# Kernel tuning notes

Measured on AMD Instinct MI355X. Metric: run time of the kernel, lower is better.

The kernel has to match this reference:

```python
import jax, jax.numpy as jnp
import numpy as np

D_MODEL = 1024
N_HEADS = 16
D_K = 64
D_FF = 4 * D_MODEL
LN_EPS = 1e-5


def _ln(x, g, b):
    mu = jnp.mean(x, axis=-1, keepdims=True)
    var = jnp.mean((x - mu) ** 2, axis=-1, keepdims=True)
    return (x - mu) * jax.lax.rsqrt(var + LN_EPS) * g + b


def setup_inputs() -> dict:
    key = jax.random.key(0)
    ks = jax.random.split(key, 24)
    d, h, dk, dff = D_MODEL, N_HEADS, D_K, D_FF
    s = lambda k, sh, fan: jax.random.normal(k, sh, jnp.float32) / np.sqrt(fan)
    return {
        "x": jax.random.normal(ks[0], (2, 2048, d), jnp.float32),
        "mask": jnp.ones((2, 2048), jnp.int32),
        # pre-attention q/k/v embed linears (d -> d)
        "Wqe": s(ks[1], (d, d), d), "bqe": jnp.zeros((d,), jnp.float32),
        "Wke": s(ks[2], (d, d), d), "bke": jnp.zeros((d,), jnp.float32),
        "Wve": s(ks[3], (d, d), d), "bve": jnp.zeros((d,), jnp.float32),
        # MHA projections (d -> h*dk) and output fc
        "Wq": s(ks[4], (d, h * dk), d), "bq": jnp.zeros((h * dk,), jnp.float32),
        "Wk": s(ks[5], (d, h * dk), d), "bk": jnp.zeros((h * dk,), jnp.float32),
        "Wv": s(ks[6], (d, h * dk), d), "bv": jnp.zeros((h * dk,), jnp.float32),
        "Wo": s(ks[7], (h * dk, d), h * dk), "bo": jnp.zeros((d,), jnp.float32),
        # layer norms
        "g1": jnp.ones((d,), jnp.float32), "b1": jnp.zeros((d,), jnp.float32),
        "g2": jnp.ones((d,), jnp.float32), "b2": jnp.zeros((d,), jnp.float32),
        # FFN
        "W1": s(ks[8], (d, dff), d), "bb1": jnp.zeros((dff,), jnp.float32),
        "W2": s(ks[9], (dff, d), dff), "bb2": jnp.zeros((d,), jnp.float32),
    }


def reference(x, mask, Wqe, bqe, Wke, bke, Wve, bve, Wq, bq, Wk, bk, Wv, bv,
              Wo, bo, g1, b1, g2, b2, W1, bb1, W2, bb2):
    N, T, _ = x.shape
    h, dk = N_HEADS, D_K
    # pre-embeds then MHA projections
    q = ((x @ Wqe + bqe) @ Wq + bq).reshape(N, T, h, dk)
    k = ((x @ Wke + bke) @ Wk + bk).reshape(N, T, h, dk)
    v = ((x @ Wve + bve) @ Wv + bv).reshape(N, T, h, dk)
    scores = jnp.einsum("bthd,bshd->bhts", q, k) / np.sqrt(dk).astype(np.float32)
    scores = jnp.where(mask[:, None, None, :] == 0, -jnp.inf, scores)
    attn = jax.nn.softmax(scores, axis=-1)
    a = jnp.einsum("bhts,bshd->bthd", attn, v).reshape(N, T, h * dk)
    mha_out = a @ Wo + bo
    x = _ln(x + mha_out, g1, b1)
    ffn = jax.nn.gelu(x @ W1 + bb1, approximate=False) @ W2 + bb2
    x = _ln(x + ffn, g2, b2)
    return x  # dropout is identity in eval mode
```

## Files before the change

### kernel.cpp

```cpp
#include <hip/hip_runtime.h>
#include <stdint.h>
#include <math.h>


#define DM   1024
#define DFF  4096
#define NH   16
#define DKH  64
#define TSEQ 2048
#define TOK  4096

using f32x4  = float  __attribute__((ext_vector_type(4)));
using bf16x8 = __bf16 __attribute__((ext_vector_type(8)));
using s16x8  = short  __attribute__((ext_vector_type(8)));

typedef const void __attribute__((address_space(1)))* gas_ptr;
typedef void       __attribute__((address_space(3)))* las_ptr;

__device__ __forceinline__ short f2bf(float f) {
  unsigned u; __builtin_memcpy(&u, &f, 4);
  u += 0x7FFFu + ((u >> 16) & 1u);
  return (short)(u >> 16);
}
__device__ __forceinline__ float bf2f(short s) {
  unsigned u = ((unsigned)(unsigned short)s) << 16;
  float f; __builtin_memcpy(&f, &u, 4);
  return f;
}
__device__ __forceinline__ unsigned cvt_pk_bf16(float lo, float hi) {
  unsigned r;
  asm volatile("v_cvt_pk_bf16_f32 %0, %1, %2" : "=v"(r) : "v"(lo), "v"(hi));
  return r;
}
__device__ __forceinline__ f32x4 mfma16(s16x8 a, s16x8 b, f32x4 c) {
  return __builtin_amdgcn_mfma_f32_16x16x32_bf16(
      __builtin_bit_cast(bf16x8, a), __builtin_bit_cast(bf16x8, b), c, 0, 0, 0);
}
__device__ __forceinline__ void gload16(const void* g, void* l) {
  __builtin_amdgcn_global_load_lds((gas_ptr)g, (las_ptr)l, 16, 0, 0);
}
__device__ __forceinline__ float gelu_f(float x) {
  float u = x * (0.7978845608f + 0.0356774081f * x * x);
  float e = exp2f(u * 2.8853900818f);
  return x - x / (1.f + e);
}

struct CvtArgs { const float* S[4]; short* D[4]; long n[4]; };
__global__ void cvt_bf16_b(CvtArgs a) {
  const int z = blockIdx.y;
  long i = ((long)blockIdx.x * 256 + threadIdx.x) * 8;
  if (i >= a.n[z]) return;
  const float* S = a.S[z]; short* D = a.D[z];
  float4 va = *(const float4*)(S + i);
  float4 vb = *(const float4*)(S + i + 4);
  s16x8 o;
  o[0]=f2bf(va.x); o[1]=f2bf(va.y); o[2]=f2bf(va.z); o[3]=f2bf(va.w);
  o[4]=f2bf(vb.x); o[5]=f2bf(vb.y); o[6]=f2bf(vb.z); o[7]=f2bf(vb.w);
  *(s16x8*)(D + i) = o;
}

struct TcvtArgs { const float* W[4]; short* WT[4]; };
template<int NZ>
__global__ __launch_bounds__(256) void transpose_cvt(TcvtArgs a, int R, int C) {
  __shared__ float t[64][65];
  const int z = (NZ > 1) ? blockIdx.z : 0;
  const float* __restrict__ W = a.W[z];
  short* __restrict__ WT = a.WT[z];
  const int c0 = blockIdx.x * 64, r0 = blockIdx.y * 64;
  const int tr = threadIdx.x >> 4, tc = (threadIdx.x & 15) * 4;
  #pragma unroll
  for (int q = 0; q < 4; q++) {
    int rr = q * 16 + tr;
    float4 v = *(const float4*)(W + (long)(r0 + rr) * C + c0 + tc);
    t[rr][tc] = v.x; t[rr][tc+1] = v.y; t[rr][tc+2] = v.z; t[rr][tc+3] = v.w;
  }
  __syncthreads();
  #pragma unroll
  for (int q = 0; q < 4; q++) {
    int rr = q * 16 + tr;
    short4 o;
    o.x = f2bf(t[tc+0][rr]); o.y = f2bf(t[tc+1][rr]);
    o.z = f2bf(t[tc+2][rr]); o.w = f2bf(t[tc+3][rr]);
    *(short4*)(WT + (long)(c0 + rr) * R + r0 + tc) = o;
  }
}

struct BiasArgs {
  const float* be[3]; const short* WT[3]; const float* b2[3]; float* bc[3]; int K;
};
__global__ void fuse_bias(BiasArgs a) {
  const int z = blockIdx.y, n = blockIdx.x, lane = threadIdx.x;
  const float* be = a.be[z];
  const short* WT = a.WT[z] + (long)n * a.K;
  float s = 0.f;
  for (int k = lane; k < a.K; k += 64) s += be[k] * bf2f(WT[k]);
  #pragma unroll
  for (int d = 1; d < 64; d <<= 1) s += __shfl_xor(s, d);
  if (lane == 0) a.bc[z][n] = s + a.b2[z][n];
}

struct GemmArgs {
  const short* A[3]; const short* B[3]; const float* bias[3]; void* C[6];
  float oscale[3];
  int M, N, K;
  int tmask;
  int zshift;
};

template<int EPI>
__global__ __launch_bounds__(256) void gemm_bt(GemmArgs g) {
  const int zz = blockIdx.z;
  const int prob = zz >> g.zshift;
  const int slice = zz & ((1 << g.zshift) - 1);
  const short* __restrict__ A = g.A[prob];
  const short* __restrict__ B = g.B[prob];
  const float* __restrict__ bias = g.bias[prob];
  const int N = g.N, K = g.K;
  const int Ks = K >> g.zshift;
  const int kbase = slice * Ks;
  const int tn = blockIdx.x * 128, tm = blockIdx.y * 128;
  const int tid = threadIdx.x;
  const int lane = tid & 63, w = tid >> 6;
  const int wr = w >> 1, wc = w & 1;
  const int g2 = lane >> 4, q = lane & 15;

  __shared__ alignas(16) short lbuf[2][128 * 64];
  short* lA = &lbuf[0][0];
  short* lB = &lbuf[1][0];

  f32x4 acc[4][4] = {};

  const int srow = lane >> 3;
  const int scol = lane & 7;

  for (int k0 = 0; k0 < Ks; k0 += 64) {
    #pragma unroll
    for (int qq = 0; qq < 4; qq++) {
      const int row  = w * 32 + qq * 8 + srow;
      const int slot = scol ^ (row & 7);
      gload16(A + (long)(tm + row) * K + kbase + k0 + slot * 8,
              lA + (w * 32 + qq * 8) * 64);
      gload16(B + (long)(tn + row) * K + kbase + k0 + slot * 8,
              lB + (w * 32 + qq * 8) * 64);
    }
    __syncthreads();
    #pragma unroll
    for (int kk = 0; kk < 2; kk++) {
      s16x8 af[4], bfr[4];
      #pragma unroll
      for (int m = 0; m < 4; m++) {
        const int row = wr * 64 + m * 16 + q;
        const int ps  = (kk * 4 + g2) ^ (row & 7);
        af[m] = *(const s16x8*)(lA + row * 64 + ps * 8);
      }
      #pragma unroll
      for (int n = 0; n < 4; n++) {
        const int row = wc * 64 + n * 16 + q;
        const int ps  = (kk * 4 + g2) ^ (row & 7);
        bfr[n] = *(const s16x8*)(lB + row * 64 + ps * 8);
      }
      #pragma unroll
      for (int m = 0; m < 4; m++)
        #pragma unroll
        for (int n = 0; n < 4; n++)
          acc[m][n] = mfma16(af[m], bfr[n], acc[m][n]);
    }
    __syncthreads();
  }

  const bool outT = (g.tmask >> prob) & 1;
  const float sc = g.oscale[prob];
  float bv[4];
  #pragma unroll
  for (int n = 0; n < 4; n++)
    bv[n] = bias ? bias[tn + wc * 64 + n * 16 + q] : 0.f;

  if (EPI == 1) {
    float* C = (float*)g.C[zz];
    #pragma unroll
    for (int n = 0; n < 4; n++) {
      const int col = tn + wc * 64 + n * 16 + q;
      #pragma unroll
      for (int m = 0; m < 4; m++) {
        const int row0 = tm + wr * 64 + m * 16 + g2 * 4;
        #pragma unroll
        for (int r = 0; r < 4; r++)
          C[(long)(row0 + r) * N + col] = (acc[m][n][r] + bv[n]) * sc;
      }
    }
  } else {
    short* lC = &lbuf[0][0];
    short* C = (short*)g.C[zz];
    #pragma unroll
    for (int h2 = 0; h2 < 2; h2++) {
      __syncthreads();
      if (!outT ? (wr == h2) : (wc == h2)) {
        #pragma unroll
        for (int m = 0; m < 4; m++)
          #pragma unroll
          for (int n = 0; n < 4; n++)
            #pragma unroll
            for (int r = 0; r < 4; r++) {
              float xv = (acc[m][n][r] + bv[n]) * sc;
              if (EPI == 2) xv = gelu_f(xv);
              if (!outT) {
                const int rl = m * 16 + g2 * 4 + r;
                const int cl = wc * 64 + n * 16 + q;
                lC[rl * 136 + cl] = f2bf(xv);
              } else {
                const int cl = n * 16 + q;
                const int rl = wr * 64 + m * 16 + g2 * 4 + r;
                lC[cl * 136 + rl] = f2bf(xv);
              }
            }
      }
      __syncthreads();
      const int lrow = tid >> 4, l16 = tid & 15;
      #pragma unroll
      for (int rr = 0; rr < 4; rr++) {
        const int row = rr * 16 + lrow;
        s16x8 vv = *(const s16x8*)(lC + row * 136 + l16 * 8);
        if (!outT)
          *(s16x8*)(C + (long)(tm + h2 * 64 + row) * N + tn + l16 * 8) = vv;
        else
          *(s16x8*)(C + (long)(tn + h2 * 64 + row) * g.M + tm + l16 * 8) = vv;
      }
    }
  }
}

__global__ __launch_bounds__(256) void flash_attn(const short* __restrict__ Q,
                                                  const short* __restrict__ Km,
                                                  const short* __restrict__ VT,
                                                  const int* __restrict__ mask,
                                                  short* __restrict__ O) {
  const int qt = blockIdx.x;
  const int bh = blockIdx.y;
  const int b = bh >> 4, h = bh & 15;
  const int lane = threadIdx.x & 63, w = threadIdx.x >> 6;
  const int g2 = lane >> 4, q = lane & 15;

  __shared__ alignas(16) short lK[2][64 * 64];
  __shared__ alignas(16) short lV[2][64 * 64];
  __shared__ alignas(16) short lP[4][16 * 64];

  const int qrow0 = b * TSEQ + qt * 64 + w * 16;

  s16x8 qf[2];
  #pragma unroll
  for (int kk = 0; kk < 2; kk++)
    qf[kk] = *(const s16x8*)(Q + (long)(qrow0 + q) * DM + h * DKH + kk * 32 + g2 * 8);

  float lI = 0.f;
  f32x4 oacc[4] = {};

  const int srow = lane >> 3, scol = lane & 7;
  short* lPw = &lP[w][0];
  const int psw = (q & 7) << 3;

  const int nt = TSEQ / 64;
  #pragma unroll
  for (int t2 = 0; t2 < 2; t2++) {
    const int row  = w * 16 + t2 * 8 + srow;
    const int slot = scol ^ (row & 7);
    gload16(Km + (long)(b * TSEQ + row) * DM + h * DKH + slot * 8,
            &lK[0][(w * 16 + t2 * 8) * 64]);
    gload16(VT + (long)(h * DKH + row) * TOK + b * TSEQ + slot * 8,
            &lV[0][(w * 16 + t2 * 8) * 64]);
  }

  for (int t = 0; t < nt; t++) {
    const int cb = t & 1;
    const short* lKc = &lK[cb][0];
    const short* lVc = &lV[cb][0];
    __syncthreads();

    if (t + 1 < nt) {
      const int kvn = (t + 1) * 64;
      #pragma unroll
      for (int t2 = 0; t2 < 2; t2++) {
        const int row  = w * 16 + t2 * 8 + srow;
        const int slot = scol ^ (row & 7);
        gload16(Km + (long)(b * TSEQ + kvn + row) * DM + h * DKH + slot * 8,
                &lK[cb ^ 1][(w * 16 + t2 * 8) * 64]);
        gload16(VT + (long)(h * DKH + row) * TOK + b * TSEQ + kvn + slot * 8,
                &lV[cb ^ 1][(w * 16 + t2 * 8) * 64]);
      }
    }
    const int mk = mask[b * TSEQ + t * 64 + lane];

    f32x4 s[4] = {};
    __builtin_amdgcn_s_setprio(1);
    #pragma unroll
    for (int kk = 0; kk < 2; kk++)
      #pragma unroll
      for (int n = 0; n < 4; n++) {
        const int row = n * 16 + q;
        const int ps  = (kk * 4 + g2) ^ (row & 7);
        s16x8 kf = *(const s16x8*)(lKc + row * 64 + ps * 8);
        s[n] = mfma16(kf, qf[kk], s[n]);
      }
    __builtin_amdgcn_s_setprio(0);

    float p[4][4];
    #pragma unroll
    for (int n = 0; n < 4; n++)
      #pragma unroll
      for (int r = 0; r < 4; r++)
        p[n][r] = exp2f(s[n][r]);

    if (__ballot(mk == 0)) {
      const float mzf = mk ? 1.f : 0.f;
      #pragma unroll
      for (int n = 0; n < 4; n++)
        #pragma unroll
        for (int r = 0; r < 4; r++)
          p[n][r] *= __shfl(mzf, n * 16 + g2 * 4 + r);
    }
    #pragma unroll
    for (int n = 0; n < 4; n++)
      lI += (p[n][0] + p[n][1]) + (p[n][2] + p[n][3]);

    #pragma unroll
    for (int n = 0; n < 4; n++)
      #pragma unroll
      for (int hh = 0; hh < 2; hh++) {
        unsigned pk = cvt_pk_bf16(p[n][2 * hh], p[n][2 * hh + 1]);
        *(unsigned*)(lPw + ((q * 64 + n * 16 + g2 * 4 + 2 * hh) ^ psw)) = pk;
      }
    s16x8 pf[2];
    #pragma unroll
    for (int kk = 0; kk < 2; kk++)
      pf[kk] = *(const s16x8*)(lPw + ((q * 64 + kk * 32 + g2 * 8) ^ psw));

    __builtin_amdgcn_s_setprio(1);
    #pragma unroll
    for (int kk = 0; kk < 2; kk++)
      #pragma unroll
      for (int n = 0; n < 4; n++) {
        const int row = n * 16 + q;
        const int ps  = (kk * 4 + g2) ^ (row & 7);
        s16x8 vf = *(const s16x8*)(lVc + row * 64 + ps * 8);
        oacc[n] = mfma16(pf[kk], vf, oacc[n]);
      }
    __builtin_amdgcn_s_setprio(0);
  }

  lI += __shfl_xor(lI, 16);
  lI += __shfl_xor(lI, 32);
  float rI[4];
  #pragma unroll
  for (int r = 0; r < 4; r++) rI[r] = 1.f / __shfl(lI, g2 * 4 + r);
  #pragma unroll
  for (int n = 0; n < 4; n++) {
    const int col = h * DKH + n * 16 + q;
    #pragma unroll
    for (int r = 0; r < 4; r++) {
      const int row = qrow0 + g2 * 4 + r;
      O[(long)row * DM + col] = f2bf(oacc[n][r] * rI[r]);
    }
  }
}

template<bool WB16>
__global__ __launch_bounds__(256) void ln_residual(const float* __restrict__ X,
                                                   const float* __restrict__ P0,
                                                   const float* __restrict__ P1,
                                                   const float* __restrict__ rbias,
                                                   const float* __restrict__ gw,
                                                   const float* __restrict__ bw,
                                                   float* __restrict__ Yf,
                                                   short* __restrict__ Yb) {
  const int row = blockIdx.x, tid = threadIdx.x;
  const float4 xv = *(const float4*)(X + (long)row * DM + tid * 4);
  const float4 p0 = *(const float4*)(P0 + (long)row * DM + tid * 4);
  const float4 p1 = *(const float4*)(P1 + (long)row * DM + tid * 4);
  const float4 rb = *(const float4*)(rbias + tid * 4);
  float v[4] = {xv.x + p0.x + p1.x + rb.x, xv.y + p0.y + p1.y + rb.y,
                xv.z + p0.z + p1.z + rb.z, xv.w + p0.w + p1.w + rb.w};
  float s  = v[0] + v[1] + v[2] + v[3];
  float s2 = v[0]*v[0] + v[1]*v[1] + v[2]*v[2] + v[3]*v[3];
  #pragma unroll
  for (int d = 1; d < 64; d <<= 1) { s += __shfl_xor(s, d); s2 += __shfl_xor(s2, d); }
  __shared__ float red[8];
  const int lane = tid & 63, w = tid >> 6;
  if (lane == 0) { red[w] = s; red[w + 4] = s2; }
  __syncthreads();
  s  = red[0] + red[1] + red[2] + red[3];
  s2 = red[4] + red[5] + red[6] + red[7];
  const float mu  = s * (1.f / DM);
  const float inv = rsqrtf(s2 * (1.f / DM) - mu * mu + 1e-5f);
  #pragma unroll
  for (int i = 0; i < 4; i++) {
    const int col = tid * 4 + i;
    const float y = (v[i] - mu) * inv * gw[col] + bw[col];
    Yf[(long)row * DM + col] = y;
    if (WB16) Yb[(long)row * DM + col] = f2bf(y);
  }
}

extern "C" void kernel_launch(void* const* d_in, const int* in_sizes, int n_in,
                              void* d_out, int out_size, void* d_ws, size_t ws_size,
                              hipStream_t stream) {
  const float* x   = (const float*)d_in[0];
  const int*   msk = (const int*)d_in[1];
  const float* Wqe = (const float*)d_in[2];  const float* bqe = (const float*)d_in[3];
  const float* Wke = (const float*)d_in[4];  const float* bke = (const float*)d_in[5];
  const float* Wve = (const float*)d_in[6];  const float* bve = (const float*)d_in[7];
  const float* Wq  = (const float*)d_in[8];  const float* bq  = (const float*)d_in[9];
  const float* Wk  = (const float*)d_in[10]; const float* bk  = (const float*)d_in[11];
  const float* Wv  = (const float*)d_in[12]; const float* bv  = (const float*)d_in[13];
  const float* Wo  = (const float*)d_in[14]; const float* bo  = (const float*)d_in[15];
  const float* g1  = (const float*)d_in[16]; const float* b1  = (const float*)d_in[17];
  const float* g2  = (const float*)d_in[18]; const float* b2  = (const float*)d_in[19];
  const float* W1  = (const float*)d_in[20]; const float* bb1 = (const float*)d_in[21];
  const float* W2  = (const float*)d_in[22]; const float* bb2 = (const float*)d_in[23];

  char* ws = (char*)d_ws;
  const size_t MB = 1024ull * 1024ull;
  short* xb   = (short*)(ws + 0);
  short* woT  = (short*)(ws + 8 * MB);
  short* w1T  = (short*)(ws + 10 * MB);
  short* w2T  = (short*)(ws + 18 * MB);
  short* wqeB = (short*)(ws + 26 * MB);
  short* wkeB = (short*)(ws + 28 * MB);
  short* wveB = (short*)(ws + 30 * MB);
  short* wqT  = (short*)(ws + 32 * MB);
  short* wkT  = (short*)(ws + 34 * MB);
  short* wvT  = (short*)(ws + 36 * MB);
  short* wcqT = (short*)(ws + 38 * MB);
  short* wckT = (short*)(ws + 40 * MB);
  short* wcvT = (short*)(ws + 42 * MB);
  float* bcq  = (float*)(ws + 44 * MB);
  float* bck  = (float*)(ws + 44 * MB + 16384);
  float* bcv  = (float*)(ws + 44 * MB + 32768);
  short* Qb   = (short*)(ws + 45 * MB);
  short* Kb2  = (short*)(ws + 53 * MB);
  short* VTb  = (short*)(ws + 61 * MB);
  float* mhaP0= (float*)(ws + 26 * MB);
  float* mhaP1= (float*)(ws + 42 * MB);
  short* Hb   = (short*)(ws + 26 * MB);
  float* yf   = (float*)(ws + 58 * MB);
  short* ybf  = (short*)(ws + 74 * MB);
  float* ffnP0= (float*)d_out;
  float* ffnP1= (float*)(ws + 0);
  short* Aout = xb;

  CvtArgs ca = {};
  ca.S[0] = x;  ca.D[0] = xb;   ca.n[0] = (long)TOK * DM;
  ca.S[1] = Wqe; ca.D[1] = wqeB; ca.n[1] = (long)DM * DM;
  ca.S[2] = Wke; ca.D[2] = wkeB; ca.n[2] = (long)DM * DM;
  ca.S[3] = Wve; ca.D[3] = wveB; ca.n[3] = (long)DM * DM;
  cvt_bf16_b<<<dim3((long)TOK * DM / 2048, 4), 256, 0, stream>>>(ca);

  TcvtArgs t4 = {};
  t4.W[0] = Wq; t4.WT[0] = wqT;  t4.W[1] = Wk; t4.WT[1] = wkT;
  t4.W[2] = Wv; t4.WT[2] = wvT;  t4.W[3] = Wo; t4.WT[3] = woT;
  transpose_cvt<4><<<dim3(16, 16, 4), 256, 0, stream>>>(t4, DM, DM);
  TcvtArgs t1 = {}; t1.W[0] = W1; t1.WT[0] = w1T;
  transpose_cvt<1><<<dim3(64, 16), 256, 0, stream>>>(t1, DM, DFF);
  TcvtArgs t2 = {}; t2.W[0] = W2; t2.WT[0] = w2T;
  transpose_cvt<1><<<dim3(16, 64), 256, 0, stream>>>(t2, DFF, DM);

  GemmArgs fa = {};
  fa.A[0] = wqT;  fa.A[1] = wkT;  fa.A[2] = wvT;
  fa.B[0] = wqeB; fa.B[1] = wkeB; fa.B[2] = wveB;
  fa.C[0] = wcqT; fa.C[1] = wckT; fa.C[2] = wcvT;
  fa.oscale[0] = 1.f; fa.oscale[1] = 1.f; fa.oscale[2] = 1.f;
  fa.M = DM; fa.N = DM; fa.K = DM; fa.tmask = 0; fa.zshift = 0;
  gemm_bt<0><<<dim3(8, 8, 3), 256, 0, stream>>>(fa);

  BiasArgs ba = {};
  ba.be[0] = bqe; ba.be[1] = bke; ba.be[2] = bve;
  ba.WT[0] = wqT; ba.WT[1] = wkT; ba.WT[2] = wvT;
  ba.b2[0] = bq;  ba.b2[1] = bk;  ba.b2[2] = bv;
  ba.bc[0] = bcq; ba.bc[1] = bck; ba.bc[2] = bcv; ba.K = DM;
  fuse_bias<<<dim3(DM, 3), 64, 0, stream>>>(ba);

  GemmArgs qa = {};
  qa.A[0] = xb;   qa.A[1] = xb;   qa.A[2] = xb;
  qa.B[0] = wcqT; qa.B[1] = wckT; qa.B[2] = wcvT;
  qa.bias[0] = bcq; qa.bias[1] = bck; qa.bias[2] = bcv;
  qa.C[0] = Qb; qa.C[1] = Kb2; qa.C[2] = VTb;
  qa.oscale[0] = 0.125f * 1.44269504f; qa.oscale[1] = 1.f; qa.oscale[2] = 1.f;
  qa.M = TOK; qa.N = DM; qa.K = DM; qa.tmask = 4; qa.zshift = 0;
  gemm_bt<0><<<dim3(8, 32, 3), 256, 0, stream>>>(qa);

  flash_attn<<<dim3(TSEQ / 64, 2 * NH), 256, 0, stream>>>(Qb, Kb2, VTb, msk, Aout);

  GemmArgs oa = {};
  oa.A[0] = Aout; oa.B[0] = woT; oa.bias[0] = nullptr;
  oa.C[0] = mhaP0; oa.C[1] = mhaP1;
  oa.oscale[0] = 1.f;
  oa.M = TOK; oa.N = DM; oa.K = DM; oa.tmask = 0; oa.zshift = 1;
  gemm_bt<1><<<dim3(8, 32, 2), 256, 0, stream>>>(oa);

  ln_residual<true><<<dim3(TOK), 256, 0, stream>>>(x, mhaP0, mhaP1, bo,
                                                   g1, b1, yf, ybf);

  GemmArgs f1 = {};
  f1.A[0] = ybf; f1.B[0] = w1T; f1.bias[0] = bb1; f1.C[0] = Hb;
  f1.oscale[0] = 1.f;
  f1.M = TOK; f1.N = DFF; f1.K = DM; f1.tmask = 0; f1.zshift = 0;
  gemm_bt<2><<<dim3(32, 32, 1), 256, 0, stream>>>(f1);

  GemmArgs f2 = {};
  f2.A[0] = Hb; f2.B[0] = w2T; f2.bias[0] = nullptr;
  f2.C[0] = ffnP0; f2.C[1] = ffnP1;
  f2.oscale[0] = 1.f;
  f2.M = TOK; f2.N = DM; f2.K = DFF; f2.tmask = 0; f2.zshift = 1;
  gemm_bt<1><<<dim3(8, 32, 2), 256, 0, stream>>>(f2);

  ln_residual<false><<<dim3(TOK), 256, 0, stream>>>(yf, ffnP0, ffnP1, bb2,
                                                    g2, b2, (float*)d_out, nullptr);
}
```

Baseline: 315.4 us.

## Add 256x256-tile 512-thread GEMM kernel for QKV and FFN1 projections

```diff
diff --git a/kernel.cpp b/kernel.cpp
--- a/kernel.cpp
+++ b/kernel.cpp
@@ -225,6 +225,139 @@
         else
           *(s16x8*)(C + (long)(tn + h2 * 64 + row) * g.M + tm + l16 * 8) = vv;
       }
+    }
+  }
+}
+
+struct Gemm256Args {
+  const short* A[3]; const short* B[3]; const float* bias[3]; void* C[3];
+  float oscale[3];
+  int M, N, K;
+  int tmask;
+};
+
+template<int EPI>
+__global__ __launch_bounds__(512, 2) void gemm256(Gemm256Args g) {
+  const int prob = blockIdx.z;
+  const short* __restrict__ A = g.A[prob];
+  const short* __restrict__ B = g.B[prob];
+  const float* __restrict__ bias = g.bias[prob];
+  const int N = g.N, K = g.K;
+
+  const int gx = gridDim.x;
+  const int nwg = gx * gridDim.y;
+  const int bid = blockIdx.y * gx + blockIdx.x;
+  const int cpx = nwg >> 3;
+  const int tile = (bid & 7) * cpx + (bid >> 3);
+  const int tn = (tile % gx) * 256, tm = (tile / gx) * 256;
+
+  const int tid = threadIdx.x;
+  const int lane = tid & 63, w = tid >> 6;
+  const int wr = w >> 2, wc = w & 3;
+  const int g2 = lane >> 4, q = lane & 15;
+  const int srow = lane >> 3, scol = lane & 7;
+
+  __shared__ alignas(16) short lA[2][256 * 64];
+  __shared__ alignas(16) short lB[2][256 * 64];
+
+  f32x4 acc[8][4] = {};
+
+  auto STAGE = [&](int kb, int bf) {
+    #pragma unroll
+    for (int qq = 0; qq < 4; qq++) {
+      const int row  = w * 32 + qq * 8 + srow;
+      const int slot = scol ^ (row & 7);
+      gload16(A + (long)(tm + row) * K + kb + slot * 8, &lA[bf][(w * 32 + qq * 8) * 64]);
+      gload16(B + (long)(tn + row) * K + kb + slot * 8, &lB[bf][(w * 32 + qq * 8) * 64]);
+    }
+  };
+
+  STAGE(0, 0);
+  __syncthreads();
+
+  const int nk = K >> 6;
+  for (int it = 0; it < nk; it++) {
+    const int cur = it & 1;
+    if (it + 1 < nk) STAGE((it + 1) << 6, cur ^ 1);
+
+    const short* cA = &lA[cur][0];
+    const short* cB = &lB[cur][0];
+    s16x8 bfr[4][2];
+    #pragma unroll
+    for (int n = 0; n < 4; n++)
+      #pragma unroll
+      for (int kk = 0; kk < 2; kk++) {
+        const int row = wc * 64 + n * 16 + q;
+        const int ps  = (kk * 4 + g2) ^ (row & 7);
+        bfr[n][kk] = *(const s16x8*)(cB + row * 64 + ps * 8);
+      }
+    __builtin_amdgcn_s_setprio(1);
+    #pragma unroll
+    for (int m = 0; m < 8; m++) {
+      s16x8 af[2];
+      #pragma unroll
+      for (int kk = 0; kk < 2; kk++) {
+        const int row = wr * 128 + m * 16 + q;
+        const int ps  = (kk * 4 + g2) ^ (row & 7);
+        af[kk] = *(const s16x8*)(cA + row * 64 + ps * 8);
+      }
+      #pragma unroll
+      for (int kk = 0; kk < 2; kk++)
+        #pragma unroll
+        for (int n = 0; n < 4; n++)
+          acc[m][n] = mfma16(af[kk], bfr[n][kk], acc[m][n]);
+    }
+    __builtin_amdgcn_s_setprio(0);
+    __syncthreads();
+  }
+
+  short* lC = &lA[0][0];
+  short* C = (short*)g.C[prob];
+  const bool outT = (g.tmask >> prob) & 1;
+  const float sc = g.oscale[prob];
+  float bv[4];
+  #pragma unroll
+  for (int n = 0; n < 4; n++)
+    bv[n] = bias ? bias[tn + wc * 64 + n * 16 + q] : 0.f;
+
+  for (int p = 0; p < 4; p++) {
+    __syncthreads();
+    if (!outT) {
+      if (wr == (p >> 1)) {
+        const int mb = (p & 1) * 4;
+        #pragma unroll
+        for (int mm = 0; mm < 4; mm++)
+          #pragma unroll
+          for (int n = 0; n < 4; n++)
+            #pragma unroll
+            for (int r = 0; r < 4; r++) {
+              float xv = (acc[mb + mm][n][r] + bv[n]) * sc;
+              if (EPI == 2) xv = gelu_f(xv);
+              lC[(mm * 16 + g2 * 4 + r) * 272 + wc * 64 + n * 16 + q] = f2bf(xv);
+            }
+      }
+    } else {
+      if (wc == p) {
+        #pragma unroll
+        for (int m = 0; m < 8; m++)
+          #pragma unroll
+          for (int n = 0; n < 4; n++)
+            #pragma unroll
+            for (int r = 0; r < 4; r++) {
+              float xv = (acc[m][n][r] + bv[n]) * sc;
+              lC[(n * 16 + q) * 272 + wr * 128 + m * 16 + g2 * 4 + r] = f2bf(xv);
+            }
+      }
+    }
+    __syncthreads();
+    #pragma unroll
+    for (int rr = 0; rr < 4; rr++) {
+      const int row = rr * 16 + (tid >> 5);
+      s16x8 vv = *(const s16x8*)(lC + row * 272 + (tid & 31) * 8);
+      if (!outT)
+        *(s16x8*)(C + (long)(tm + p * 64 + row) * N + tn + (tid & 31) * 8) = vv;
+      else
+        *(s16x8*)(C + (long)(tn + p * 64 + row) * g.M + tm + (tid & 31) * 8) = vv;
     }
   }
 }
@@ -477,14 +610,14 @@
   ba.bc[0] = bcq; ba.bc[1] = bck; ba.bc[2] = bcv; ba.K = DM;
   fuse_bias<<<dim3(DM, 3), 64, 0, stream>>>(ba);
 
-  GemmArgs qa = {};
+  Gemm256Args qa = {};
   qa.A[0] = xb;   qa.A[1] = xb;   qa.A[2] = xb;
   qa.B[0] = wcqT; qa.B[1] = wckT; qa.B[2] = wcvT;
   qa.bias[0] = bcq; qa.bias[1] = bck; qa.bias[2] = bcv;
   qa.C[0] = Qb; qa.C[1] = Kb2; qa.C[2] = VTb;
   qa.oscale[0] = 0.125f * 1.44269504f; qa.oscale[1] = 1.f; qa.oscale[2] = 1.f;
-  qa.M = TOK; qa.N = DM; qa.K = DM; qa.tmask = 4; qa.zshift = 0;
-  gemm_bt<0><<<dim3(8, 32, 3), 256, 0, stream>>>(qa);
+  qa.M = TOK; qa.N = DM; qa.K = DM; qa.tmask = 4;
+  gemm256<0><<<dim3(4, 16, 3), 512, 0, stream>>>(qa);
 
   flash_attn<<<dim3(TSEQ / 64, 2 * NH), 256, 0, stream>>>(Qb, Kb2, VTb, msk, Aout);
 
@@ -498,11 +631,11 @@
   ln_residual<true><<<dim3(TOK), 256, 0, stream>>>(x, mhaP0, mhaP1, bo,
                                                    g1, b1, yf, ybf);
 
-  GemmArgs f1 = {};
+  Gemm256Args f1 = {};
   f1.A[0] = ybf; f1.B[0] = w1T; f1.bias[0] = bb1; f1.C[0] = Hb;
   f1.oscale[0] = 1.f;
-  f1.M = TOK; f1.N = DFF; f1.K = DM; f1.tmask = 0; f1.zshift = 0;
-  gemm_bt<2><<<dim3(32, 32, 1), 256, 0, stream>>>(f1);
+  f1.M = TOK; f1.N = DFF; f1.K = DM; f1.tmask = 0;
+  gemm256<2><<<dim3(16, 16, 1), 512, 0, stream>>>(f1);
 
   GemmArgs f2 = {};
   f2.A[0] = Hb; f2.B[0] = w2T; f2.bias[0] = nullptr;
```

Result: slower. 937.8 us (+197.4%).
